# Kernel optimization log

Hardware: AMD Instinct MI355X
Metric: run time of the kernel (lower is better)

The kernel has to match this reference:

```python
import jax, jax.numpy as jnp
import numpy as np

P, K, N, D = 4, 3, 250000, 64  # n_paths, num_powers, n_nodes, dim
N_EDGES = 100000


def setup_inputs() -> dict:
    key = jax.random.key(0)
    k1, k2, k3, k4 = jax.random.split(key, 4)
    feats = jax.random.normal(k1, (P, K, N, D), dtype=jnp.float32)
    # Each (path, power) slice was L2-normalized per node row in the original.
    feats = feats / jnp.linalg.norm(feats, axis=-1, keepdims=True)
    feature_weights = jnp.ones((P, K), dtype=jnp.float32)  # nn.Parameter init = ones
    intercept = jnp.float32(0.0)
    idx_i = jax.random.randint(k2, (N_EDGES,), 0, N, dtype=jnp.int64)
    idx_j = jax.random.randint(k3, (N_EDGES,), 0, N, dtype=jnp.int64)
    return {
        "precomputed_features": feats,
        "feature_weights": feature_weights,
        "intercept": intercept,
        "idx_i": idx_i,
        "idx_j": idx_j,
    }


def reference(precomputed_features, feature_weights, intercept, idx_i, idx_j):
    # softmax over the num_powers axis (dim=1 in torch)
    w = jax.nn.softmax(feature_weights, axis=1)  # [P, K]
    # weighted sum over paths and powers -> [N, D] embedding table
    emb = jnp.einsum("pk,pknd->nd", w, precomputed_features)
    zi = emb[idx_i]  # [E, D]
    zj = emb[idx_j]  # [E, D]
    dim = precomputed_features.shape[-1]
    dist_sq = jnp.sum((zi - zj) ** 2, axis=-1)
    logits = intercept - dist_sq / dim
    return jax.nn.sigmoid(logits)
```

## Files before the change

kernel.cpp:

```cpp
#include <hip/hip_runtime.h>
#include <math.h>


constexpr int Pp = 4;
constexpr int Kk = 3;
constexpr int Nn = 250000;
constexpr int Dd = 64;
constexpr int PK = Pp * Kk;

__device__ __forceinline__ void softmax_weights(const float* __restrict__ fw,
                                                float* __restrict__ w) {
    #pragma unroll
    for (int p = 0; p < Pp; ++p) {
        float e[Kk];
        float m = -INFINITY;
        #pragma unroll
        for (int k = 0; k < Kk; ++k) {
            e[k] = fw[p * Kk + k];
            m = fmaxf(m, e[k]);
        }
        float s = 0.0f;
        #pragma unroll
        for (int k = 0; k < Kk; ++k) {
            e[k] = __expf(e[k] - m);
            s += e[k];
        }
        const float inv = 1.0f / s;
        #pragma unroll
        for (int k = 0; k < Kk; ++k) w[p * Kk + k] = e[k] * inv;
    }
}

__global__ __launch_bounds__(256) void fastrp_emb_kernel(
    const float* __restrict__ feats,
    const float* __restrict__ fw,
    float*       __restrict__ emb,
    int total4)
{
    float w[PK];
    softmax_weights(fw, w);

    const int stride = gridDim.x * blockDim.x;
    for (int v = blockIdx.x * blockDim.x + threadIdx.x; v < total4; v += stride) {
        float4 acc = make_float4(0.0f, 0.0f, 0.0f, 0.0f);
        #pragma unroll
        for (int pk = 0; pk < PK; ++pk) {
            const float4* src =
                reinterpret_cast<const float4*>(feats + (size_t)pk * Nn * Dd);
            const float4 f = src[v];
            acc.x = fmaf(w[pk], f.x, acc.x);
            acc.y = fmaf(w[pk], f.y, acc.y);
            acc.z = fmaf(w[pk], f.z, acc.z);
            acc.w = fmaf(w[pk], f.w, acc.w);
        }
        reinterpret_cast<float4*>(emb)[v] = acc;
    }
}

__global__ __launch_bounds__(256) void fastrp_edge_from_emb(
    const float* __restrict__ emb,
    const float* __restrict__ intercept,
    const int*   __restrict__ idx_i,
    const int*   __restrict__ idx_j,
    float*       __restrict__ out,
    int E)
{
    const int tid  = (int)(blockIdx.x * blockDim.x + threadIdx.x);
    const int lane = threadIdx.x & 63;
    const int q    = lane & 15;
    const int e    = tid >> 4;
    if (e >= E) return;

    const long long i = (long long)idx_i[e];
    const long long j = (long long)idx_j[e];

    const float4 zi = *reinterpret_cast<const float4*>(emb + i * Dd + q * 4);
    const float4 zj = *reinterpret_cast<const float4*>(emb + j * Dd + q * 4);

    const float dx = zi.x - zj.x;
    const float dy = zi.y - zj.y;
    const float dz = zi.z - zj.z;
    const float dw = zi.w - zj.w;
    float v = dx * dx + dy * dy + dz * dz + dw * dw;

    v += __shfl_xor(v, 1, 64);
    v += __shfl_xor(v, 2, 64);
    v += __shfl_xor(v, 4, 64);
    v += __shfl_xor(v, 8, 64);

    if (q == 0) {
        const float logit = intercept[0] - v * (1.0f / Dd);
        out[e] = 1.0f / (1.0f + __expf(-logit));
    }
}

__global__ __launch_bounds__(256) void fastrp_edge_kernel(
    const float* __restrict__ feats, const float* __restrict__ fw,
    const float* __restrict__ intercept, const int* __restrict__ idx_i,
    const int* __restrict__ idx_j, float* __restrict__ out, int E)
{
    const int wave = (int)((blockIdx.x * (size_t)blockDim.x + threadIdx.x) >> 6);
    const int lane = threadIdx.x & 63;
    if (wave >= E) return;

    float w[PK];
    softmax_weights(fw, w);

    const long long i = (long long)idx_i[wave];
    const long long j = (long long)idx_j[wave];

    float zi = 0.0f, zj = 0.0f;
    #pragma unroll
    for (int pk = 0; pk < PK; ++pk) {
        const float* base = feats + (size_t)pk * Nn * Dd;
        zi = fmaf(w[pk], base[i * Dd + lane], zi);
        zj = fmaf(w[pk], base[j * Dd + lane], zj);
    }

    float diff = zi - zj;
    float v = diff * diff;
    #pragma unroll
    for (int off = 32; off > 0; off >>= 1) v += __shfl_xor(v, off, 64);

    if (lane == 0) {
        const float logit = intercept[0] - v * (1.0f / Dd);
        out[wave] = 1.0f / (1.0f + __expf(-logit));
    }
}

extern "C" void kernel_launch(void* const* d_in, const int* in_sizes, int n_in,
                              void* d_out, int out_size, void* d_ws, size_t ws_size,
                              hipStream_t stream) {
    const float* feats     = (const float*)d_in[0];
    const float* fw        = (const float*)d_in[1];
    const float* intercept = (const float*)d_in[2];
    const int*   idx_i     = (const int*)d_in[3];
    const int*   idx_j     = (const int*)d_in[4];
    float*       out       = (float*)d_out;

    const int E = in_sizes[3];
    const size_t emb_bytes = (size_t)Nn * Dd * sizeof(float);

    if (ws_size >= emb_bytes) {
        float* emb = (float*)d_ws;

        const int total4 = Nn * Dd / 4;
        const int block1 = 256;
        const int grid1  = 2048;
        fastrp_emb_kernel<<<grid1, block1, 0, stream>>>(feats, fw, emb, total4);

        const int block2 = 256;
        const int edges_per_block = block2 / 16;
        const int grid2 = (E + edges_per_block - 1) / edges_per_block;
        fastrp_edge_from_emb<<<grid2, block2, 0, stream>>>(emb, intercept,
                                                           idx_i, idx_j, out, E);
    } else {
        const int block = 256;
        const int waves_per_block = block / 64;
        const int grid = (E + waves_per_block - 1) / waves_per_block;
        fastrp_edge_kernel<<<grid, block, 0, stream>>>(feats, fw, intercept,
                                                       idx_i, idx_j, out, E);
    }
}
```

Before: 984.5 us.

## Compute embeddings only for nodes referenced by edges via bitmap

Builds a bitmap of nodes referenced by idx_i/idx_j using atomicOr, then computes the weighted embedding only for marked nodes instead of all 250k. This cuts the full streaming read of the 12 feature slices (about 768 MB) to roughly the touched fraction, about 55% of nodes with 200k random indices. It adds two small kernels (zero, build) and atomic traffic. Reads still come as row-granular 256-byte chunks, so coalescing within a row is kept.

New measurement: 924.6 us. 1.06x faster.

```diff
diff --git a/kernel.cpp b/kernel.cpp
--- a/kernel.cpp
+++ b/kernel.cpp
@@ -7,6 +7,9 @@
 constexpr int Nn = 250000;
 constexpr int Dd = 64;
 constexpr int PK = Pp * Kk;
+constexpr int BM_WORDS = (Nn + 31) / 32;
+
+typedef float v4f __attribute__((ext_vector_type(4)));
 
 __device__ __forceinline__ void softmax_weights(const float* __restrict__ fw,
                                                 float* __restrict__ w) {
@@ -31,30 +34,49 @@
     }
 }
 
-__global__ __launch_bounds__(256) void fastrp_emb_kernel(
+__global__ __launch_bounds__(256) void bm_zero(unsigned int* __restrict__ bm) {
+    const int t = blockIdx.x * blockDim.x + threadIdx.x;
+    if (t < BM_WORDS) bm[t] = 0u;
+}
+
+__global__ __launch_bounds__(256) void bm_build(const int* __restrict__ idx_i,
+                                                const int* __restrict__ idx_j,
+                                                unsigned int* __restrict__ bm,
+                                                int E) {
+    const int t = blockIdx.x * blockDim.x + threadIdx.x;
+    if (t >= E) return;
+    const int a = idx_i[t];
+    const int b = idx_j[t];
+    atomicOr(&bm[a >> 5], 1u << (a & 31));
+    atomicOr(&bm[b >> 5], 1u << (b & 31));
+}
+
+__global__ __launch_bounds__(256) void fastrp_emb_touched(
     const float* __restrict__ feats,
     const float* __restrict__ fw,
-    float*       __restrict__ emb,
-    int total4)
+    const unsigned int* __restrict__ bm,
+    float*       __restrict__ emb)
 {
+    const int t = blockIdx.x * blockDim.x + threadIdx.x;
+    const int n = t >> 4;
+    const int q = t & 15;
+    if (n >= Nn) return;
+    if (!((bm[n >> 5] >> (n & 31)) & 1u)) return;
+
     float w[PK];
     softmax_weights(fw, w);
 
-    const int stride = gridDim.x * blockDim.x;
-    for (int v = blockIdx.x * blockDim.x + threadIdx.x; v < total4; v += stride) {
-        float4 acc = make_float4(0.0f, 0.0f, 0.0f, 0.0f);
-        #pragma unroll
-        for (int pk = 0; pk < PK; ++pk) {
-            const float4* src =
-                reinterpret_cast<const float4*>(feats + (size_t)pk * Nn * Dd);
-            const float4 f = src[v];
-            acc.x = fmaf(w[pk], f.x, acc.x);
-            acc.y = fmaf(w[pk], f.y, acc.y);
-            acc.z = fmaf(w[pk], f.z, acc.z);
-            acc.w = fmaf(w[pk], f.w, acc.w);
-        }
-        reinterpret_cast<float4*>(emb)[v] = acc;
+    const size_t off = (size_t)n * Dd + q * 4;
+    v4f acc = 0.0f;
+    #pragma unroll
+    for (int pk = 0; pk < PK; ++pk) {
+        const v4f f = *reinterpret_cast<const v4f*>(feats + (size_t)pk * Nn * Dd + off);
+        acc.x = fmaf(w[pk], f.x, acc.x);
+        acc.y = fmaf(w[pk], f.y, acc.y);
+        acc.z = fmaf(w[pk], f.z, acc.z);
+        acc.w = fmaf(w[pk], f.w, acc.w);
     }
+    *reinterpret_cast<v4f*>(emb + off) = acc;
 }
 
 __global__ __launch_bounds__(256) void fastrp_edge_from_emb(
@@ -66,8 +88,7 @@
     int E)
 {
     const int tid  = (int)(blockIdx.x * blockDim.x + threadIdx.x);
-    const int lane = threadIdx.x & 63;
-    const int q    = lane & 15;
+    const int q    = threadIdx.x & 15;
     const int e    = tid >> 4;
     if (e >= E) return;
 
@@ -140,24 +161,25 @@
 
     const int E = in_sizes[3];
     const size_t emb_bytes = (size_t)Nn * Dd * sizeof(float);
+    const size_t need = emb_bytes + (size_t)BM_WORDS * sizeof(unsigned int);
 
-    if (ws_size >= emb_bytes) {
+    if (ws_size >= need) {
         float* emb = (float*)d_ws;
+        unsigned int* bm = (unsigned int*)((char*)d_ws + emb_bytes);
 
-        const int total4 = Nn * Dd / 4;
-        const int block1 = 256;
-        const int grid1  = 2048;
-        fastrp_emb_kernel<<<grid1, block1, 0, stream>>>(feats, fw, emb, total4);
+        bm_zero<<<(BM_WORDS + 255) / 256, 256, 0, stream>>>(bm);
+        bm_build<<<(E + 255) / 256, 256, 0, stream>>>(idx_i, idx_j, bm, E);
 
-        const int block2 = 256;
-        const int edges_per_block = block2 / 16;
-        const int grid2 = (E + edges_per_block - 1) / edges_per_block;
-        fastrp_edge_from_emb<<<grid2, block2, 0, stream>>>(emb, intercept,
-                                                           idx_i, idx_j, out, E);
+        const int threads1 = Nn * 16;
+        fastrp_emb_touched<<<(threads1 + 255) / 256, 256, 0, stream>>>(
+            feats, fw, bm, emb);
+
+        const int threads2 = E * 16;
+        fastrp_edge_from_emb<<<(threads2 + 255) / 256, 256, 0, stream>>>(
+            emb, intercept, idx_i, idx_j, out, E);
     } else {
         const int block = 256;
-        const int waves_per_block = block / 64;
-        const int grid = (E + waves_per_block - 1) / waves_per_block;
+        const int grid = (E + block / 64 - 1) / (block / 64);
         fastrp_edge_kernel<<<grid, block, 0, stream>>>(feats, fw, intercept,
                                                        idx_i, idx_j, out, E);
     }
```
